# Kernel optimization log

Hardware: AMD Instinct MI355X
Metric: run time of the kernel (lower is better)

## Reference

```python
import jax, jax.numpy as jnp
import numpy as np

NZ, NX, NT, NS, NR = 150, 300, 1000, 4, 400
DX, DT, FREQ = 10.0, 0.001, 15.0
# 8th-order central-difference coefficients for the 2nd derivative
C = (-205.0 / 72.0, 8.0 / 5.0, -1.0 / 5.0, 8.0 / 315.0, -1.0 / 560.0)
HALO = 4


def setup_inputs() -> dict:
    key = jax.random.key(0)
    k1, k2 = jax.random.split(key, 2)
    # velocity model in [1500, 3500] m/s
    v_map = (1500.0 + 2000.0 * jax.random.uniform(k1, (NZ, NX))).astype(jnp.float32)
    # Ricker wavelet source, slightly perturbed per shot
    t = jnp.arange(NT, dtype=jnp.float32) * DT - 1.0 / FREQ
    a = (jnp.pi * FREQ * t) ** 2
    ricker = (1.0 - 2.0 * a) * jnp.exp(-a)
    s_amp = (ricker[None, :] * (1.0 + 0.01 * jax.random.normal(k2, (NS, NT)))).astype(jnp.float32)
    # sources: shallow depth, spread in x
    sz = jnp.full((NS,), 5, dtype=jnp.int32)
    sx = jnp.round(jnp.linspace(20, NX - 21, NS)).astype(jnp.int32)
    s_loc = jnp.stack([sz, sx], axis=-1)
    # receivers: near-surface line
    rz = jnp.full((NR,), 2, dtype=jnp.int32)
    rx = jnp.round(jnp.linspace(HALO, NX - 1 - HALO, NR)).astype(jnp.int32)
    r_loc = jnp.stack([rz, rx], axis=-1)
    return {"v_map": v_map, "s_amp": s_amp, "s_loc": s_loc, "r_loc": r_loc}


def _laplacian(u, nz, nx):
    # u: [S, nz, nx]; zero-padded 8th-order 5-point-per-axis stencil
    up = jnp.pad(u, ((0, 0), (HALO, HALO), (HALO, HALO)))
    out = 2.0 * C[0] * u
    for k in range(1, 5):
        out = out + C[k] * (
            up[:, HALO + k:HALO + k + nz, HALO:HALO + nx]
            + up[:, HALO - k:HALO - k + nz, HALO:HALO + nx]
            + up[:, HALO:HALO + nz, HALO + k:HALO + k + nx]
            + up[:, HALO:HALO + nz, HALO - k:HALO - k + nx]
        )
    return out / (DX * DX)


def reference(v_map, s_amp, s_loc, r_loc):
    nz, nx = v_map.shape
    ns = s_amp.shape[0]
    sz, sx = s_loc[:, 0], s_loc[:, 1]
    rz, rx = r_loc[:, 0], r_loc[:, 1]
    shot_ids = jnp.arange(ns)
    v2dt2 = (v_map * DT) ** 2                      # [nz, nx]
    src_scale = v2dt2[sz, sx]                      # [ns]

    def step(carry, amp_t):
        u_prev, u_cur = carry                      # each [ns, nz, nx]
        u_next = 2.0 * u_cur - u_prev + v2dt2[None] * _laplacian(u_cur, nz, nx)
        u_next = u_next.at[shot_ids, sz, sx].add(src_scale * amp_t)
        rec = u_next[:, rz, rx]                    # [ns, n_rec]
        return (u_cur, u_next), rec

    u0 = jnp.zeros((ns, nz, nx), dtype=v_map.dtype)
    _, recs = jax.lax.scan(step, (u0, u0), s_amp.T)  # recs: [nt, ns, n_rec]
    rec_gth = jnp.transpose(recs, (1, 0, 2))         # [ns, nt, n_rec]
    return rec_gth
```

## Files before the change

kernel.cpp:

```cpp
#include <hip/hip_runtime.h>


#define NZ_ 150
#define NX_ 300
#define NT_ 1000
#define NS_ 4
#define NR_ 400
#define KS_ 8
#define NCH_ 9
#define NBND_ 8
#define HW_ 32
#define ZW_ 168
#define LROWS_ 98
#define BUF_ (LROWS_*ZW_)
#define THR_ 512
#define NRND_ 125
#define HELE_ 4800
#define NBATCH 19

typedef float f4 __attribute__((ext_vector_type(4)));
typedef unsigned long long u64;

__device__ __forceinline__ void astore64(u64* p, u64 v) {
    __hip_atomic_store(p, v, __ATOMIC_RELAXED, __HIP_MEMORY_SCOPE_AGENT);
}
__device__ __forceinline__ int aload32(const int* p) {
    return __hip_atomic_load(p, __ATOMIC_RELAXED, __HIP_MEMORY_SCOPE_AGENT);
}
__device__ __forceinline__ void astore32(int* p, int v) {
    __hip_atomic_store(p, v, __ATOMIC_RELAXED, __HIP_MEMORY_SCOPE_AGENT);
}
__device__ __forceinline__ void ld2_issue(u64& d, const u64* p) {
    asm volatile("global_load_dwordx2 %0, %1, off sc0 sc1" : "=v"(d) : "v"(p));
}
__device__ __forceinline__ int* flagp(int* flags, int s, int bnd, int dir, int wv) {
    return flags + (((s * NBND_ + bnd) * 2 + dir) * 4 + wv);
}

__global__ __launch_bounds__(THR_) void wave_pf(
    const float* __restrict__ v_map, const float* __restrict__ s_amp,
    const int* __restrict__ s_loc, const int* __restrict__ r_loc,
    float* __restrict__ out, int* __restrict__ flags, u64* __restrict__ halo)
{
    extern __shared__ float smem[];
    const int bi = blockIdx.x;
    const int s = bi & 3;
    const int h = bi >> 2;
    const int tid = threadIdx.x;

    const int w  = 33 + (h < 3 ? 1 : 0);
    const int x0 = 33 * h + (h < 3 ? h : 3);
    const int rhi = HW_ + w;

    for (int i = tid; i < 2 * BUF_; i += THR_) smem[i] = 0.0f;

    const int zg = tid % 38;
    const int xp = tid / 38;
    const bool comp = (tid < 494);
    const int c0 = 4 + 4 * zg;
    const int rbase = 8 * xp;

    f4 v2r[8];
#pragma unroll
    for (int i = 0; i < 8; ++i) {
        f4 vv = {0.f, 0.f, 0.f, 0.f};
        const int row = rbase + i;
        const int x = x0 - HW_ + row;
        if (comp && x >= 0 && x < NX_) {
#pragma unroll
            for (int j = 0; j < 4; ++j) {
                const int z = min(4 * zg + j, NZ_ - 1);
                const float v = v_map[z * NX_ + x] * 0.001f;
                vv[j] = v * v * 0.01f;
            }
        }
        v2r[i] = vv;
    }

    const int sz = s_loc[2 * s], sx = s_loc[2 * s + 1];
    float sS = v_map[sz * NX_ + sx] * 0.001f; sS = sS * sS;
    const int srow = sx - x0 + HW_;
    const int szg = sz >> 2;
    const int scol = 4 + sz;

    bool rown = false; int rrow = 0, rcol = 0;
    if (tid < NR_) {
        const int rz = r_loc[2 * tid];
        const int rx = r_loc[2 * tid + 1];
        if (rx >= x0 && rx < x0 + w) { rown = true; rrow = HW_ + rx - x0; rcol = 4 + rz; }
    }

    __syncthreads();

    for (int r = 0; r < NRND_; ++r) {
        for (int k = 1; k <= KS_; ++k) {
            const int tau = KS_ * r + k;
            const int ext = 4 * (KS_ - k);
            const int L  = (h == 0)        ? HW_ : HW_ - ext;
            const int R  = (h == NCH_ - 1) ? rhi : rhi + ext;
            const float* cur = smem + ((tau + 1) & 1) * BUF_;
            float*       nxt = smem + (tau & 1) * BUF_;

            if (comp && rbase < R && rbase + 8 > L) {
                f4 W[9];
#pragma unroll
                for (int q = 0; q < 8; ++q) {
                    int rr = rbase - 4 + q; rr = rr < 0 ? 0 : rr;
                    W[q] = *(const f4*)&cur[rr * ZW_ + c0];
                }
#pragma unroll
                for (int i = 0; i < 8; ++i) {
                    const int row = rbase + i;
                    const int wr = (row + 4 < LROWS_) ? (row + 4) : (LROWS_ - 1);
                    W[8] = *(const f4*)&cur[wr * ZW_ + c0];
                    if (row >= L && row < R) {
                        const f4 lf = *(const f4*)&cur[row * ZW_ + c0 - 4];
                        const f4 rt = *(const f4*)&cur[row * ZW_ + c0 + 4];
                        const f4 pv = *(const f4*)&nxt[row * ZW_ + c0];
                        float xw[12];
#pragma unroll
                        for (int j = 0; j < 4; ++j) { xw[j] = lf[j]; xw[4 + j] = W[4][j]; xw[8 + j] = rt[j]; }
                        f4 res;
#pragma unroll
                        for (int j = 0; j < 4; ++j) {
                            const float ct = xw[4 + j];
                            float lap = 2.0f * (-205.0f / 72.0f) * ct;
                            lap += (8.0f / 5.0f)    * ((xw[j + 3] + xw[j + 5]) + (W[3][j] + W[5][j]));
                            lap += (-1.0f / 5.0f)   * ((xw[j + 2] + xw[j + 6]) + (W[2][j] + W[6][j]));
                            lap += (8.0f / 315.0f)  * ((xw[j + 1] + xw[j + 7]) + (W[1][j] + W[7][j]));
                            lap += (-1.0f / 560.0f) * ((xw[j + 0] + xw[j + 8]) + (W[0][j] + W[8][j]));
                            res[j] = 2.0f * ct - pv[j] + v2r[i][j] * lap;
                        }
                        if (zg != 37) {
                            *(f4*)&nxt[row * ZW_ + c0] = res;
                        } else {
                            nxt[row * ZW_ + c0]     = res[0];
                            nxt[row * ZW_ + c0 + 1] = res[1];
                        }
                        if (row == srow && zg == szg)
                            nxt[row * ZW_ + scol] += sS * s_amp[s * NT_ + tau - 1];
                    }
#pragma unroll
                    for (int q = 0; q < 8; ++q) W[q] = W[q + 1];
                }
            }
            __syncthreads();
            if (rown) {
                const float* nb = smem + (tau & 1) * BUF_;
                out[((size_t)s * NT_ + (tau - 1)) * NR_ + tid] = nb[rrow * ZW_ + rcol];
            }
        }

        if (r < NRND_ - 1) {
            const int par = r & 1;
            const int wv  = (tid & 255) >> 6;
            if (tid < 256) {
                if (h > 0) {
                    u64* dst = halo + (size_t)(((s * NBND_ + h - 1) * 2 + 1) * 2 + par) * HELE_;
                    for (int e = tid; e < HELE_; e += 256) {
                        const int f = e / 2400, rem = e - f * 2400, row = rem / 75, zp = rem - row * 75;
                        astore64(dst + e, *(const u64*)&smem[f * BUF_ + (HW_ + row) * ZW_ + 4 + 2 * zp]);
                    }
                    asm volatile("s_waitcnt vmcnt(0)" ::: "memory");
                    if ((tid & 63) == 0)
                        astore32(flagp(flags, s, h - 1, 1, wv), r + 1);
                }
            } else {
                if (h < NCH_ - 1) {
                    u64* dst = halo + (size_t)(((s * NBND_ + h) * 2 + 0) * 2 + par) * HELE_;
                    for (int e = tid - 256; e < HELE_; e += 256) {
                        const int f = e / 2400, rem = e - f * 2400, row = rem / 75, zp = rem - row * 75;
                        astore64(dst + e, *(const u64*)&smem[f * BUF_ + (w + row) * ZW_ + 4 + 2 * zp]);
                    }
                    asm volatile("s_waitcnt vmcnt(0)" ::: "memory");
                    if ((tid & 63) == 0)
                        astore32(flagp(flags, s, h, 0, wv), r + 1);
                }
            }
            if (tid < 256) {
                if (h > 0) {
                    const int* fp = flagp(flags, s, h - 1, 0, wv);
                    while (aload32(fp) <= r) __builtin_amdgcn_s_sleep(1);
                    const u64* src = halo + (size_t)(((s * NBND_ + h - 1) * 2 + 0) * 2 + par) * HELE_;
                    u64 vb[NBATCH];
#pragma unroll
                    for (int q = 0; q < NBATCH; ++q) {
                        const int e = tid + 256 * q;
                        ld2_issue(vb[q], src + (e < HELE_ ? e : HELE_ - 1));
                    }
                    asm volatile("s_waitcnt vmcnt(0)" ::: "memory");
                    __builtin_amdgcn_sched_barrier(0);
#pragma unroll
                    for (int q = 0; q < NBATCH; ++q) {
                        const int e = tid + 256 * q;
                        if (e < HELE_) {
                            const int f = e / 2400, rem = e - f * 2400, row = rem / 75, zp = rem - row * 75;
                            *(u64*)&smem[f * BUF_ + row * ZW_ + 4 + 2 * zp] = vb[q];
                        }
                    }
                }
            } else {
                if (h < NCH_ - 1) {
                    const int* fp = flagp(flags, s, h, 1, wv);
                    while (aload32(fp) <= r) __builtin_amdgcn_s_sleep(1);
                    const u64* src = halo + (size_t)(((s * NBND_ + h) * 2 + 1) * 2 + par) * HELE_;
                    u64 vb[NBATCH];
#pragma unroll
                    for (int q = 0; q < NBATCH; ++q) {
                        const int e = (tid - 256) + 256 * q;
                        ld2_issue(vb[q], src + (e < HELE_ ? e : HELE_ - 1));
                    }
                    asm volatile("s_waitcnt vmcnt(0)" ::: "memory");
                    __builtin_amdgcn_sched_barrier(0);
#pragma unroll
                    for (int q = 0; q < NBATCH; ++q) {
                        const int e = (tid - 256) + 256 * q;
                        if (e < HELE_) {
                            const int f = e / 2400, rem = e - f * 2400, row = rem / 75, zp = rem - row * 75;
                            *(u64*)&smem[f * BUF_ + (rhi + row) * ZW_ + 4 + 2 * zp] = vb[q];
                        }
                    }
                }
            }
            __syncthreads();
        }
    }
}

extern "C" void kernel_launch(void* const* d_in, const int* in_sizes, int n_in,
                              void* d_out, int out_size, void* d_ws, size_t ws_size,
                              hipStream_t stream) {
    const float* v_map = (const float*)d_in[0];
    const float* s_amp = (const float*)d_in[1];
    const int*   s_loc = (const int*)d_in[2];
    const int*   r_loc = (const int*)d_in[3];
    float* out = (float*)d_out;

    int* flags = (int*)d_ws;
    u64* halo  = (u64*)((char*)d_ws + 4096);

    hipMemsetAsync(d_ws, 0, 4096, stream);

    const int smem_bytes = 2 * BUF_ * 4;
    static bool attr_set = false;
    if (!attr_set) {
        hipFuncSetAttribute((const void*)wave_pf,
                            hipFuncAttributeMaxDynamicSharedMemorySize, smem_bytes);
        attr_set = true;
    }

    wave_pf<<<dim3(NS_ * NCH_), dim3(THR_), smem_bytes, stream>>>(
        v_map, s_amp, s_loc, r_loc, out, flags, halo);
}
```

Before: 2.918 ms.

## Split halo exchange to overlap first-frame transfer with final substep compute

```diff
diff --git a/kernel.cpp b/kernel.cpp
--- a/kernel.cpp
+++ b/kernel.cpp
@@ -13,10 +13,10 @@
 #define ZW_ 168
 #define LROWS_ 98
 #define BUF_ (LROWS_*ZW_)
-#define THR_ 512
+#define THR_ 768
 #define NRND_ 125
 #define HELE_ 4800
-#define NBATCH 19
+#define NB_H 10
 
 typedef float f4 __attribute__((ext_vector_type(4)));
 typedef unsigned long long u64;
@@ -33,14 +33,15 @@
 __device__ __forceinline__ void ld2_issue(u64& d, const u64* p) {
     asm volatile("global_load_dwordx2 %0, %1, off sc0 sc1" : "=v"(d) : "v"(p));
 }
-__device__ __forceinline__ int* flagp(int* flags, int s, int bnd, int dir, int wv) {
-    return flags + (((s * NBND_ + bnd) * 2 + dir) * 4 + wv);
-}
-
-__global__ __launch_bounds__(THR_) void wave_pf(
+__device__ __forceinline__ int* flagp(int* f, int s, int bnd, int dir, int wv) {
+    return f + (((s * NBND_ + bnd) * 2 + dir) * 4 + wv);
+}
+
+__global__ __launch_bounds__(THR_) void wave_ox(
     const float* __restrict__ v_map, const float* __restrict__ s_amp,
     const int* __restrict__ s_loc, const int* __restrict__ r_loc,
-    float* __restrict__ out, int* __restrict__ flags, u64* __restrict__ halo)
+    float* __restrict__ out, int* __restrict__ flagsA, int* __restrict__ flagsB,
+    u64* __restrict__ halo)
 {
     extern __shared__ float smem[];
     const int bi = blockIdx.x;
@@ -56,13 +57,13 @@
 
     const int zg = tid % 38;
     const int xp = tid / 38;
-    const bool comp = (tid < 494);
+    const bool comp = (tid < 760);
     const int c0 = 4 + 4 * zg;
-    const int rbase = 8 * xp;
-
-    f4 v2r[8];
-#pragma unroll
-    for (int i = 0; i < 8; ++i) {
+    const int rbase = 5 * xp;
+
+    f4 v2r[5];
+#pragma unroll
+    for (int i = 0; i < 5; ++i) {
         f4 vv = {0.f, 0.f, 0.f, 0.f};
         const int row = rbase + i;
         const int x = x0 - HW_ + row;
@@ -90,9 +91,15 @@
         if (rx >= x0 && rx < x0 + w) { rown = true; rrow = HW_ + rx - x0; rcol = 4 + rz; }
     }
 
+    const int wv   = (tid & 255) >> 6;
+    const bool sideL = (tid < 256);
+    const bool sideR = (tid >= 256 && tid < 512);
+    const int tidS = tid & 255;
+
     __syncthreads();
 
     for (int r = 0; r < NRND_; ++r) {
+        u64 vb[NB_H];
         for (int k = 1; k <= KS_; ++k) {
             const int tau = KS_ * r + k;
             const int ext = 4 * (KS_ - k);
@@ -101,7 +108,7 @@
             const float* cur = smem + ((tau + 1) & 1) * BUF_;
             float*       nxt = smem + (tau & 1) * BUF_;
 
-            if (comp && rbase < R && rbase + 8 > L) {
+            if (comp && rbase < R && rbase + 5 > L) {
                 f4 W[9];
 #pragma unroll
                 for (int q = 0; q < 8; ++q) {
@@ -109,7 +116,7 @@
                     W[q] = *(const f4*)&cur[rr * ZW_ + c0];
                 }
 #pragma unroll
-                for (int i = 0; i < 8; ++i) {
+                for (int i = 0; i < 5; ++i) {
                     const int row = rbase + i;
                     const int wr = (row + 4 < LROWS_) ? (row + 4) : (LROWS_ - 1);
                     W[8] = *(const f4*)&cur[wr * ZW_ + c0];
@@ -149,75 +156,125 @@
                 const float* nb = smem + (tau & 1) * BUF_;
                 out[((size_t)s * NT_ + (tau - 1)) * NR_ + tid] = nb[rrow * ZW_ + rcol];
             }
+
+            if (k == 7 && r < NRND_ - 1) {
+                const int par = r & 1;
+                if (sideL && h > 0) {
+                    u64* dst = halo + (size_t)(((s * NBND_ + h - 1) * 2 + 1) * 2 + par) * HELE_ + 2400;
+                    for (int e = tidS; e < 2400; e += 256) {
+                        const int row = e / 75, zp = e - row * 75;
+                        astore64(dst + e, *(const u64*)&smem[BUF_ + (HW_ + row) * ZW_ + 4 + 2 * zp]);
+                    }
+                    asm volatile("s_waitcnt vmcnt(0)" ::: "memory");
+                    if ((tid & 63) == 0) astore32(flagp(flagsA, s, h - 1, 1, wv), r + 1);
+                } else if (sideR && h < NCH_ - 1) {
+                    u64* dst = halo + (size_t)(((s * NBND_ + h) * 2 + 0) * 2 + par) * HELE_ + 2400;
+                    for (int e = tidS; e < 2400; e += 256) {
+                        const int row = e / 75, zp = e - row * 75;
+                        astore64(dst + e, *(const u64*)&smem[BUF_ + (w + row) * ZW_ + 4 + 2 * zp]);
+                    }
+                    asm volatile("s_waitcnt vmcnt(0)" ::: "memory");
+                    if ((tid & 63) == 0) astore32(flagp(flagsA, s, h, 0, wv), r + 1);
+                }
+                if (sideL && h > 0) {
+                    const int* fp = flagp(flagsA, s, h - 1, 0, wv);
+                    while (aload32(fp) <= r) __builtin_amdgcn_s_sleep(1);
+                    const u64* src = halo + (size_t)(((s * NBND_ + h - 1) * 2 + 0) * 2 + par) * HELE_ + 2400;
+#pragma unroll
+                    for (int q = 0; q < NB_H; ++q) {
+                        const int e = tidS + 256 * q;
+                        ld2_issue(vb[q], src + (e < 2400 ? e : 2399));
+                    }
+                } else if (sideR && h < NCH_ - 1) {
+                    const int* fp = flagp(flagsA, s, h, 1, wv);
+                    while (aload32(fp) <= r) __builtin_amdgcn_s_sleep(1);
+                    const u64* src = halo + (size_t)(((s * NBND_ + h) * 2 + 1) * 2 + par) * HELE_ + 2400;
+#pragma unroll
+                    for (int q = 0; q < NB_H; ++q) {
+                        const int e = tidS + 256 * q;
+                        ld2_issue(vb[q], src + (e < 2400 ? e : 2399));
+                    }
+                }
+            }
         }
 
         if (r < NRND_ - 1) {
             const int par = r & 1;
-            const int wv  = (tid & 255) >> 6;
-            if (tid < 256) {
-                if (h > 0) {
+            if (tid < 512) {
+                asm volatile("s_waitcnt vmcnt(0)" ::: "memory");
+                __builtin_amdgcn_sched_barrier(0);
+                if (sideL && h > 0) {
+#pragma unroll
+                    for (int q = 0; q < NB_H; ++q) {
+                        const int e = tidS + 256 * q;
+                        if (e < 2400) {
+                            const int row = e / 75, zp = e - row * 75;
+                            *(u64*)&smem[BUF_ + row * ZW_ + 4 + 2 * zp] = vb[q];
+                        }
+                    }
+                } else if (sideR && h < NCH_ - 1) {
+#pragma unroll
+                    for (int q = 0; q < NB_H; ++q) {
+                        const int e = tidS + 256 * q;
+                        if (e < 2400) {
+                            const int row = e / 75, zp = e - row * 75;
+                            *(u64*)&smem[BUF_ + (rhi + row) * ZW_ + 4 + 2 * zp] = vb[q];
+                        }
+                    }
+                }
+                if (sideL && h > 0) {
                     u64* dst = halo + (size_t)(((s * NBND_ + h - 1) * 2 + 1) * 2 + par) * HELE_;
-                    for (int e = tid; e < HELE_; e += 256) {
-                        const int f = e / 2400, rem = e - f * 2400, row = rem / 75, zp = rem - row * 75;
-                        astore64(dst + e, *(const u64*)&smem[f * BUF_ + (HW_ + row) * ZW_ + 4 + 2 * zp]);
-                    }
-                    asm volatile("s_waitcnt vmcnt(0)" ::: "memory");
-                    if ((tid & 63) == 0)
-                        astore32(flagp(flags, s, h - 1, 1, wv), r + 1);
-                }
-            } else {
-                if (h < NCH_ - 1) {
+                    for (int e = tidS; e < 2400; e += 256) {
+                        const int row = e / 75, zp = e - row * 75;
+                        astore64(dst + e, *(const u64*)&smem[(HW_ + row) * ZW_ + 4 + 2 * zp]);
+                    }
+                    asm volatile("s_waitcnt vmcnt(0)" ::: "memory");
+                    if ((tid & 63) == 0) astore32(flagp(flagsB, s, h - 1, 1, wv), r + 1);
+                } else if (sideR && h < NCH_ - 1) {
                     u64* dst = halo + (size_t)(((s * NBND_ + h) * 2 + 0) * 2 + par) * HELE_;
-                    for (int e = tid - 256; e < HELE_; e += 256) {
-                        const int f = e / 2400, rem = e - f * 2400, row = rem / 75, zp = rem - row * 75;
-                        astore64(dst + e, *(const u64*)&smem[f * BUF_ + (w + row) * ZW_ + 4 + 2 * zp]);
-                    }
-                    asm volatile("s_waitcnt vmcnt(0)" ::: "memory");
-                    if ((tid & 63) == 0)
-                        astore32(flagp(flags, s, h, 0, wv), r + 1);
-                }
-            }
-            if (tid < 256) {
-                if (h > 0) {
-                    const int* fp = flagp(flags, s, h - 1, 0, wv);
+                    for (int e = tidS; e < 2400; e += 256) {
+                        const int row = e / 75, zp = e - row * 75;
+                        astore64(dst + e, *(const u64*)&smem[(w + row) * ZW_ + 4 + 2 * zp]);
+                    }
+                    asm volatile("s_waitcnt vmcnt(0)" ::: "memory");
+                    if ((tid & 63) == 0) astore32(flagp(flagsB, s, h, 0, wv), r + 1);
+                }
+                if (sideL && h > 0) {
+                    const int* fp = flagp(flagsB, s, h - 1, 0, wv);
                     while (aload32(fp) <= r) __builtin_amdgcn_s_sleep(1);
                     const u64* src = halo + (size_t)(((s * NBND_ + h - 1) * 2 + 0) * 2 + par) * HELE_;
-                    u64 vb[NBATCH];
-#pragma unroll
-                    for (int q = 0; q < NBATCH; ++q) {
-                        const int e = tid + 256 * q;
-                        ld2_issue(vb[q], src + (e < HELE_ ? e : HELE_ - 1));
+#pragma unroll
+                    for (int q = 0; q < NB_H; ++q) {
+                        const int e = tidS + 256 * q;
+                        ld2_issue(vb[q], src + (e < 2400 ? e : 2399));
                     }
                     asm volatile("s_waitcnt vmcnt(0)" ::: "memory");
                     __builtin_amdgcn_sched_barrier(0);
 #pragma unroll
-                    for (int q = 0; q < NBATCH; ++q) {
-                        const int e = tid + 256 * q;
-                        if (e < HELE_) {
-                            const int f = e / 2400, rem = e - f * 2400, row = rem / 75, zp = rem - row * 75;
-                            *(u64*)&smem[f * BUF_ + row * ZW_ + 4 + 2 * zp] = vb[q];
-                        }
-                    }
-                }
-            } else {
-                if (h < NCH_ - 1) {
-                    const int* fp = flagp(flags, s, h, 1, wv);
+                    for (int q = 0; q < NB_H; ++q) {
+                        const int e = tidS + 256 * q;
+                        if (e < 2400) {
+                            const int row = e / 75, zp = e - row * 75;
+                            *(u64*)&smem[row * ZW_ + 4 + 2 * zp] = vb[q];
+                        }
+                    }
+                } else if (sideR && h < NCH_ - 1) {
+                    const int* fp = flagp(flagsB, s, h, 1, wv);
                     while (aload32(fp) <= r) __builtin_amdgcn_s_sleep(1);
                     const u64* src = halo + (size_t)(((s * NBND_ + h) * 2 + 1) * 2 + par) * HELE_;
-                    u64 vb[NBATCH];
-#pragma unroll
-                    for (int q = 0; q < NBATCH; ++q) {
-                        const int e = (tid - 256) + 256 * q;
-                        ld2_issue(vb[q], src + (e < HELE_ ? e : HELE_ - 1));
+#pragma unroll
+                    for (int q = 0; q < NB_H; ++q) {
+                        const int e = tidS + 256 * q;
+                        ld2_issue(vb[q], src + (e < 2400 ? e : 2399));
                     }
                     asm volatile("s_waitcnt vmcnt(0)" ::: "memory");
                     __builtin_amdgcn_sched_barrier(0);
 #pragma unroll
-                    for (int q = 0; q < NBATCH; ++q) {
-                        const int e = (tid - 256) + 256 * q;
-                        if (e < HELE_) {
-                            const int f = e / 2400, rem = e - f * 2400, row = rem / 75, zp = rem - row * 75;
-                            *(u64*)&smem[f * BUF_ + (rhi + row) * ZW_ + 4 + 2 * zp] = vb[q];
+                    for (int q = 0; q < NB_H; ++q) {
+                        const int e = tidS + 256 * q;
+                        if (e < 2400) {
+                            const int row = e / 75, zp = e - row * 75;
+                            *(u64*)&smem[(rhi + row) * ZW_ + 4 + 2 * zp] = vb[q];
                         }
                     }
                 }
@@ -236,19 +293,20 @@
     const int*   r_loc = (const int*)d_in[3];
     float* out = (float*)d_out;
 
-    int* flags = (int*)d_ws;
-    u64* halo  = (u64*)((char*)d_ws + 4096);
+    int* flagsA = (int*)d_ws;
+    int* flagsB = (int*)((char*)d_ws + 1024);
+    u64* halo   = (u64*)((char*)d_ws + 4096);
 
     hipMemsetAsync(d_ws, 0, 4096, stream);
 
     const int smem_bytes = 2 * BUF_ * 4;
     static bool attr_set = false;
     if (!attr_set) {
-        hipFuncSetAttribute((const void*)wave_pf,
+        hipFuncSetAttribute((const void*)wave_ox,
                             hipFuncAttributeMaxDynamicSharedMemorySize, smem_bytes);
         attr_set = true;
     }
 
-    wave_pf<<<dim3(NS_ * NCH_), dim3(THR_), smem_bytes, stream>>>(
-        v_map, s_amp, s_loc, r_loc, out, flags, halo);
-}
+    wave_ox<<<dim3(NS_ * NCH_), dim3(THR_), smem_bytes, stream>>>(
+        v_map, s_amp, s_loc, r_loc, out, flagsA, flagsB, halo);
+}
```

Result: slower. 3.869 ms (+32.6%).
